# Kernel optimization log

Hardware: AMD Instinct MI355X
Metric: run time of the kernel (lower is better)

## Reference

```python
import jax, jax.numpy as jnp
import numpy as np

TAU = 0.07          # contrastive temperature
GAMMA = 2.0         # focal gamma
W_FOCAL = 0.6
W_CONTRASTIVE = 0.2
IGNORE_INDEX = -100
MAX_ANCHORS = 8     # hardcoded cap in ContrastiveLoss
N_NEG_BATCHES = 4   # hardcoded other_batches[:4]


def setup_inputs() -> dict:
    key = jax.random.key(0)
    ks = jax.random.split(key, 5)
    B, M, V = 64, 128, 5003
    S, D = 200, 128
    return {
        "masked_logits": jax.random.normal(ks[0], (B, M, V), dtype=jnp.float32),
        "masked_targets": jax.random.randint(ks[1], (B, M), 0, V, dtype=jnp.int32),
        "masked_mask": jax.random.randint(ks[2], (B, M), 0, 2, dtype=jnp.int32),
        "product_embeddings": jax.random.normal(ks[3], (B, S, D), dtype=jnp.float32),
        "product_ids": jax.random.randint(ks[4], (B, S), 0, V, dtype=jnp.int32),
        "attention_mask": jnp.ones((B, S), dtype=jnp.int32),
    }


def focal_loss(logits, targets, mask):
    # logits [B,M,V] -> flatten to [B*M,V] as in torch
    B, M, V = logits.shape
    logits = logits.reshape(B * M, V)
    targets = targets.reshape(-1)
    mask = mask.reshape(-1)
    valid = (targets != IGNORE_INDEX) & (mask == 1)
    t = jnp.clip(targets, 0, None)
    logp = jax.nn.log_softmax(logits, axis=-1)
    lp = jnp.take_along_axis(logp, t[:, None], axis=1)[:, 0]  # log p_t
    pt = jnp.exp(lp)
    fl = ((1.0 - pt) ** GAMMA) * (-lp) * valid.astype(logits.dtype)
    denom = valid.sum()
    return jnp.where(denom > 0, fl.sum() / denom.astype(logits.dtype), jnp.zeros((), logits.dtype))


def contrastive_loss(emb, pids, amask):
    # emb [B,S,D]
    B, S, D = emb.shape
    norm = jnp.maximum(jnp.linalg.norm(emb, axis=-1, keepdims=True), 1e-12)
    e = emb / norm  # F.normalize
    valid = (amask == 1) & (pids > 0)  # [B,S]
    # first 4 other batch indices per b (static, matches other_batches[:4])
    others = np.stack([np.array([i for i in range(B) if i != b][:N_NEG_BATCHES]) for b in range(B)])  # [B,4]

    def per_b(eb, vb, ne, nv):
        # eb [S,D], vb [S] bool, ne [4,S,D] neighbor embeddings, nv [4,S] their validity
        n = vb.sum()
        n_anch = jnp.minimum(n // 2, MAX_ANCHORS)
        # valid positions first (in order), padded with S
        pos_sorted = jnp.sort(jnp.where(vb, jnp.arange(S), S))
        a_idx = jnp.clip(pos_sorted[:MAX_ANCHORS], 0, S - 1)
        p_idx = jnp.clip(jnp.take(pos_sorted, n_anch + jnp.arange(MAX_ANCHORS), mode="clip"), 0, S - 1)
        sel = jnp.arange(MAX_ANCHORS) < n_anch  # active anchors
        a_e = eb[a_idx]  # [8,D]
        p_e = eb[p_idx]  # [8,D]
        pos_sim = (a_e * p_e).sum(-1) / TAU  # [8]
        negs = ne.reshape(-1, D)             # [4S,D]
        nvm = nv.reshape(-1)                 # [4S]
        neg_sim = (a_e @ negs.T) / TAU       # [8,4S]
        neg_sim = jnp.where(nvm[None, :], neg_sim, -1e9)
        lse = jax.nn.logsumexp(jnp.concatenate([pos_sim[:, None], neg_sim], axis=-1), axis=-1)
        loss_b = jnp.where(sel, lse - pos_sim, 0.0).sum()
        return loss_b, n_anch

    ne = e[others]       # [B,4,S,D]
    nv = valid[others]   # [B,4,S]
    losses, n_anch = jax.vmap(per_b)(e, valid, ne, nv)
    pairs = n_anch.sum()
    return jnp.where(pairs > 0, losses.sum() / pairs.astype(e.dtype), jnp.zeros((), e.dtype))


def reference(masked_logits, masked_targets, masked_mask, product_embeddings, product_ids, attention_mask):
    focal = focal_loss(masked_logits, masked_targets, masked_mask)
    contrastive = contrastive_loss(product_embeddings, product_ids, attention_mask)
    total = W_FOCAL * focal + W_CONTRASTIVE * contrastive
    return total
```

## Files before the change

### kernel.cpp

```cpp
#include <hip/hip_runtime.h>

#define V 5003
#define SS 200
#define DD 128
#define TAU 0.07f
#define LOG2E 1.4426950408889634f
#define LN2 0.6931471805599453f
#define SHIFT 8.0f

#define WS_CS 16384
#define WS_PR 16448

#define NFB 2048

typedef float f4 __attribute__((ext_vector_type(4)));

__device__ __forceinline__ f4 ldnt4(const f4* p) {
    return __builtin_nontemporal_load(p);
}
__device__ __forceinline__ float ldnt1(const float* p) {
    return __builtin_nontemporal_load(p);
}

__global__ __launch_bounds__(256) void fused_loss_kernel(
    const float* __restrict__ logits,
    const int*   __restrict__ targets,
    const int*   __restrict__ mmask,
    const float* __restrict__ emb,
    const int*   __restrict__ pids,
    const int*   __restrict__ amask,
    float* __restrict__ ws)
{
    const int tid  = threadIdx.x;
    const int lane = tid & 63;
    const int wave = tid >> 6;

    __shared__ __align__(16) float anchors[8][DD];
    __shared__ float possim[8];
    __shared__ unsigned char validb[SS];
    __shared__ short poslist[16];
    __shared__ int   n_sh;
    __shared__ int   nanch_sh;
    __shared__ float red[4][8];
    __shared__ float contrib_sh[8];

    if (blockIdx.x < NFB) {
        const int r = blockIdx.x * 4 + wave;
        const float* rowp = logits + (size_t)r * V;

        const int p = (4 - ((r * 3) & 3)) & 3;
        const int t = 3 - p;
        const f4* b0 = (const f4*)(rowp + p);
        const float C = -SHIFT * LOG2E;

        const int tg = targets[r];
        const int mk = mmask[r];

        float h = (lane < p) ? ldnt1(rowp + lane) : -1e30f;
        float u = (lane < t) ? ldnt1(rowp + p + 5000 + lane) : -1e30f;

        f4 buf[4];
        #pragma unroll
        for (int k = 0; k < 4; ++k)
            buf[k] = ldnt4(b0 + k * 64 + lane);

        const float xt = rowp[tg < 0 ? 0 : tg];

        const int l19 = (lane < 34) ? lane : 0;

        float s0 = 0.f, s1 = 0.f, s2 = 0.f, s3 = 0.f;

        #pragma unroll
        for (int k = 0; k < 20; ++k) {
            f4 nxt;
            if (k + 4 < 20) {
                const int kk  = k + 4;
                const int idx = (kk < 19) ? (kk * 64 + lane) : (1216 + l19);
                nxt = ldnt4(b0 + idx);
            } else {
                nxt = (f4)(-1e30f);
            }
            f4 x = buf[k & 3];
            if (k == 19 && lane >= 34) x = (f4)(-1e30f);
            s0 += exp2f(fmaf(x.x, LOG2E, C));
            s1 += exp2f(fmaf(x.y, LOG2E, C));
            s2 += exp2f(fmaf(x.z, LOG2E, C));
            s3 += exp2f(fmaf(x.w, LOG2E, C));
            buf[k & 3] = nxt;
        }
        s0 += exp2f(fmaf(h, LOG2E, C)) + exp2f(fmaf(u, LOG2E, C));

        float s = (s0 + s1) + (s2 + s3);
        for (int off = 32; off; off >>= 1)
            s += __shfl_xor(s, off, 64);

        if (lane == 0) {
            bool valid = (tg != -100) && (mk == 1);
            float lse = SHIFT + log2f(s) * LN2;
            float lp  = xt - lse;
            float pt  = exp2f(lp * LOG2E);
            float om  = 1.0f - pt;
            ((float2*)ws)[r] = make_float2(valid ? (om * om * (-lp)) : 0.0f,
                                           valid ? 1.0f : 0.0f);
        }
    } else {
        const int b = blockIdx.x - NFB;

        if (tid == 0) n_sh = 0;
        __syncthreads();

        if (tid < SS) {
            int idx = b * SS + tid;
            bool v = (amask[idx] == 1) && (pids[idx] > 0);
            validb[tid] = v ? 1 : 0;
            if (v) atomicAdd(&n_sh, 1);
        }
        __syncthreads();

        if (tid == 0) {
            int cnt = 0;
            for (int s = 0; s < SS && cnt < 16; ++s)
                if (validb[s]) poslist[cnt++] = (short)s;
            for (; cnt < 16; ++cnt) poslist[cnt] = (short)(SS - 1);
            int n  = n_sh;
            int na = n / 2;
            if (na > 8) na = 8;
            nanch_sh = na;
        }
        __syncthreads();
        const int n_anch = nanch_sh;

        const float2* embb = (const float2*)(emb + (size_t)b * SS * DD);
        for (int jj = 0; jj < 2; ++jj) {
            int j = wave + jj * 4;
            if (j < n_anch) {
                int ai = poslist[j];
                int pi = poslist[n_anch + j];
                float2 a2 = embb[ai * 64 + lane];
                float2 p2 = embb[pi * 64 + lane];
                float na_ = a2.x * a2.x + a2.y * a2.y;
                float np_ = p2.x * p2.x + p2.y * p2.y;
                float dp  = a2.x * p2.x + a2.y * p2.y;
                for (int off = 32; off; off >>= 1) {
                    na_ += __shfl_xor(na_, off, 64);
                    np_ += __shfl_xor(np_, off, 64);
                    dp  += __shfl_xor(dp,  off, 64);
                }
                float rna = 1.0f / fmaxf(sqrtf(na_), 1e-12f);
                float rnp = 1.0f / fmaxf(sqrtf(np_), 1e-12f);
                anchors[j][2 * lane]     = a2.x * rna;
                anchors[j][2 * lane + 1] = a2.y * rna;
                if (lane == 0) possim[j] = dp * rna * rnp * (1.0f / TAU);
            } else {
                anchors[j][2 * lane]     = 0.0f;
                anchors[j][2 * lane + 1] = 0.0f;
                if (lane == 0) possim[j] = 0.0f;
            }
        }
        __syncthreads();

        float part[8];
        #pragma unroll
        for (int j = 0; j < 8; ++j) part[j] = 0.0f;

        for (int i = 0; i < 4; ++i) {
            int g = tid + i * 256;
            if (g < 4 * SS) {
                int ol = g / SS;
                int s  = g - ol * SS;
                int o  = (ol >= b) ? ol + 1 : ol;
                int idx = o * SS + s;
                if (amask[idx] == 1 && pids[idx] > 0) {
                    const float4* nb = (const float4*)(emb + (size_t)idx * DD);
                    float acc[8];
                    float n2 = 0.0f;
                    #pragma unroll
                    for (int j = 0; j < 8; ++j) acc[j] = 0.0f;
                    #pragma unroll 8
                    for (int c = 0; c < DD / 4; ++c) {
                        float4 x = nb[c];
                        n2 += x.x * x.x + x.y * x.y + x.z * x.z + x.w * x.w;
                        #pragma unroll
                        for (int j = 0; j < 8; ++j) {
                            float4 a = ((const float4*)anchors[j])[c];
                            acc[j] += a.x * x.x + a.y * x.y + a.z * x.z + a.w * x.w;
                        }
                    }
                    float rn = 1.0f / fmaxf(sqrtf(n2), 1e-12f);
                    #pragma unroll
                    for (int j = 0; j < 8; ++j) {
                        float sim = acc[j] * rn * (1.0f / TAU);
                        part[j] += exp2f(sim * LOG2E);
                    }
                }
            }
        }

        #pragma unroll
        for (int j = 0; j < 8; ++j)
            for (int off = 32; off; off >>= 1)
                part[j] += __shfl_xor(part[j], off, 64);
        if (lane == 0) {
            #pragma unroll
            for (int j = 0; j < 8; ++j) red[wave][j] = part[j];
        }
        __syncthreads();

        if (tid < 8) {
            int j = tid;
            float ps = possim[j];
            float S  = exp2f(ps * LOG2E) + red[0][j] + red[1][j] + red[2][j] + red[3][j];
            float lse = log2f(S) * LN2;
            contrib_sh[j] = (j < n_anch) ? (lse - ps) : 0.0f;
        }
        __syncthreads();
        if (tid == 0) {
            float lb = 0.0f;
            for (int j = 0; j < 8; ++j) lb += contrib_sh[j];
            ws[WS_CS + b] = lb;
            ws[WS_PR + b] = (float)n_anch;
        }
    }
}

__global__ __launch_bounds__(1024) void finalize_kernel(
    const float* __restrict__ ws, float* __restrict__ out)
{
    const int tid  = threadIdx.x;
    const int lane = tid & 63;
    const int wave = tid >> 6;
    __shared__ float r_fs[16], r_vc[16], r_cs[16], r_pr[16];

    const float2* f2 = (const float2*)ws;
    float fs = 0.f, vc = 0.f, cs = 0.f, pr = 0.f;
    #pragma unroll
    for (int i = 0; i < 8; ++i) {
        float2 v = f2[tid + i * 1024];
        fs += v.x; vc += v.y;
    }
    if (tid < 64) {
        cs = ws[WS_CS + tid];
        pr = ws[WS_PR + tid];
    }
    for (int off = 32; off; off >>= 1) {
        fs += __shfl_xor(fs, off, 64);
        vc += __shfl_xor(vc, off, 64);
        cs += __shfl_xor(cs, off, 64);
        pr += __shfl_xor(pr, off, 64);
    }
    if (lane == 0) { r_fs[wave] = fs; r_vc[wave] = vc; r_cs[wave] = cs; r_pr[wave] = pr; }
    __syncthreads();
    if (tid == 0) {
        float FS = 0.f, VC = 0.f;
        for (int w = 0; w < 16; ++w) { FS += r_fs[w]; VC += r_vc[w]; }
        float CS = r_cs[0], PR = r_pr[0];
        float focal = VC > 0.0f ? FS / VC : 0.0f;
        float contr = PR > 0.0f ? CS / PR : 0.0f;
        out[0] = 0.6f * focal + 0.2f * contr;
    }
}

extern "C" void kernel_launch(void* const* d_in, const int* in_sizes, int n_in,
                              void* d_out, int out_size, void* d_ws, size_t ws_size,
                              hipStream_t stream) {
    const float* logits  = (const float*)d_in[0];
    const int*   targets = (const int*)d_in[1];
    const int*   mmask   = (const int*)d_in[2];
    const float* emb     = (const float*)d_in[3];
    const int*   pids    = (const int*)d_in[4];
    const int*   amask   = (const int*)d_in[5];
    float* out = (float*)d_out;
    float* ws  = (float*)d_ws;

    hipLaunchKernelGGL(fused_loss_kernel, dim3(NFB + 64), dim3(256), 0, stream,
                       logits, targets, mmask, emb, pids, amask, ws);
    hipLaunchKernelGGL(finalize_kernel, dim3(1), dim3(1024), 0, stream, ws, out);
}
```

Measured before the change: 269.5 us.

## Process four logit rows per wave with double-buffered full-row register loads

Each wave now handles four logit rows instead of one, and the number of focal blocks drops from 2048 to 512. Each row is loaded into registers in full (20 float4 per lane), with two row buffers alternating so the next row's loads overlap the current row's exp/sum. This is meant to keep more memory requests in flight per wave and amortize per-block launch overhead. It costs many more VGPRs, about 160 floats per lane for the two buffers, which may lower occupancy. The (W*3)&3 alignment offset still matches each row, since 2048*i*V*3 is a multiple of 4.

Result: no change. 269.5 us (+0.0%).

```diff
diff --git a/kernel.cpp b/kernel.cpp
--- a/kernel.cpp
+++ b/kernel.cpp
@@ -11,7 +11,7 @@
 #define WS_CS 16384
 #define WS_PR 16448
 
-#define NFB 2048
+#define NFB 512
 
 typedef float f4 __attribute__((ext_vector_type(4)));
 
@@ -45,64 +45,74 @@
     __shared__ float contrib_sh[8];
 
     if (blockIdx.x < NFB) {
-        const int r = blockIdx.x * 4 + wave;
-        const float* rowp = logits + (size_t)r * V;
-
-        const int p = (4 - ((r * 3) & 3)) & 3;
+        const int W = blockIdx.x * 4 + wave;
+        const int p = (4 - ((W * 3) & 3)) & 3;
         const int t = 3 - p;
-        const f4* b0 = (const f4*)(rowp + p);
+        const int l19 = (lane < 34) ? lane : 0;
         const float C = -SHIFT * LOG2E;
 
-        const int tg = targets[r];
-        const int mk = mmask[r];
-
-        float h = (lane < p) ? ldnt1(rowp + lane) : -1e30f;
-        float u = (lane < t) ? ldnt1(rowp + p + 5000 + lane) : -1e30f;
-
-        f4 buf[4];
-        #pragma unroll
-        for (int k = 0; k < 4; ++k)
-            buf[k] = ldnt4(b0 + k * 64 + lane);
-
-        const float xt = rowp[tg < 0 ? 0 : tg];
-
-        const int l19 = (lane < 34) ? lane : 0;
-
-        float s0 = 0.f, s1 = 0.f, s2 = 0.f, s3 = 0.f;
-
-        #pragma unroll
-        for (int k = 0; k < 20; ++k) {
-            f4 nxt;
-            if (k + 4 < 20) {
-                const int kk  = k + 4;
-                const int idx = (kk < 19) ? (kk * 64 + lane) : (1216 + l19);
-                nxt = ldnt4(b0 + idx);
-            } else {
-                nxt = (f4)(-1e30f);
-            }
-            f4 x = buf[k & 3];
-            if (k == 19 && lane >= 34) x = (f4)(-1e30f);
-            s0 += exp2f(fmaf(x.x, LOG2E, C));
-            s1 += exp2f(fmaf(x.y, LOG2E, C));
-            s2 += exp2f(fmaf(x.z, LOG2E, C));
-            s3 += exp2f(fmaf(x.w, LOG2E, C));
-            buf[k & 3] = nxt;
-        }
-        s0 += exp2f(fmaf(h, LOG2E, C)) + exp2f(fmaf(u, LOG2E, C));
-
-        float s = (s0 + s1) + (s2 + s3);
-        for (int off = 32; off; off >>= 1)
-            s += __shfl_xor(s, off, 64);
-
-        if (lane == 0) {
-            bool valid = (tg != -100) && (mk == 1);
-            float lse = SHIFT + log2f(s) * LN2;
-            float lp  = xt - lse;
-            float pt  = exp2f(lp * LOG2E);
-            float om  = 1.0f - pt;
-            ((float2*)ws)[r] = make_float2(valid ? (om * om * (-lp)) : 0.0f,
-                                           valid ? 1.0f : 0.0f);
-        }
+        int tg[4], mk[4];
+        float xt[4];
+        #pragma unroll
+        for (int i = 0; i < 4; ++i) {
+            int r = W + 2048 * i;
+            tg[i] = targets[r];
+            mk[i] = mmask[r];
+        }
+        #pragma unroll
+        for (int i = 0; i < 4; ++i) {
+            const float* rp = logits + (size_t)(W + 2048 * i) * V;
+            xt[i] = rp[tg[i] < 0 ? 0 : tg[i]];
+        }
+
+        f4 A[20], B[20];
+        float hA, uA, hB, uB;
+
+        auto load_row = [&](int i, f4* buf, float& h, float& u) {
+            const float* rp = logits + (size_t)(W + 2048 * i) * V;
+            const f4* base = (const f4*)(rp + p);
+            #pragma unroll
+            for (int j = 0; j < 19; ++j)
+                buf[j] = ldnt4(base + j * 64 + lane);
+            buf[19] = ldnt4(base + 1216 + l19);
+            h = (lane < p) ? ldnt1(rp + lane) : -1e30f;
+            u = (lane < t) ? ldnt1(rp + p + 5000 + lane) : -1e30f;
+        };
+
+        auto consume_row = [&](int i, f4* buf, float h, float u) {
+            float s0 = 0.f, s1 = 0.f, s2 = 0.f, s3 = 0.f;
+            #pragma unroll
+            for (int j = 0; j < 20; ++j) {
+                f4 x = buf[j];
+                if (j == 19 && lane >= 34) x = (f4)(-1e30f);
+                s0 += exp2f(fmaf(x.x, LOG2E, C));
+                s1 += exp2f(fmaf(x.y, LOG2E, C));
+                s2 += exp2f(fmaf(x.z, LOG2E, C));
+                s3 += exp2f(fmaf(x.w, LOG2E, C));
+            }
+            s0 += exp2f(fmaf(h, LOG2E, C)) + exp2f(fmaf(u, LOG2E, C));
+            float s = (s0 + s1) + (s2 + s3);
+            for (int off = 32; off; off >>= 1)
+                s += __shfl_xor(s, off, 64);
+            if (lane == 0) {
+                bool valid = (tg[i] != -100) && (mk[i] == 1);
+                float lse = SHIFT + log2f(s) * LN2;
+                float lp  = xt[i] - lse;
+                float pt  = exp2f(lp * LOG2E);
+                float om  = 1.0f - pt;
+                ((float2*)ws)[W + 2048 * i] =
+                    make_float2(valid ? (om * om * (-lp)) : 0.0f, valid ? 1.0f : 0.0f);
+            }
+        };
+
+        load_row(0, A, hA, uA);
+        load_row(1, B, hB, uB);
+        consume_row(0, A, hA, uA);
+        load_row(2, A, hA, uA);
+        consume_row(1, B, hB, uB);
+        load_row(3, B, hB, uB);
+        consume_row(2, A, hA, uA);
+        consume_row(3, B, hB, uB);
     } else {
         const int b = blockIdx.x - NFB;
 
```
